# Kernel optimization log

Hardware: AMD Instinct MI355X
Metric: run time of the kernel (lower is better)

## Reference

```python
import jax, jax.numpy as jnp
import numpy as np

C = 64
EPS_LN = 1e-5
EPS_BN = 1e-5


def _conv1x1(x, w, b):
    # x: (B,C,H,W), w: (O,I), b: (O,)
    return jnp.einsum('oi,bihw->bohw', w, x) + b[None, :, None, None]


def _cross_attn(x_a, x_b, wq, bq, wk, bk, wv, bv):
    # query from x_a, key/value from x_b; residual onto x_a
    b, c, h, w = x_a.shape
    hw = h * w
    scale = 1.0 / jnp.sqrt(jnp.asarray(C, x_a.dtype))
    q = _conv1x1(x_a, wq, bq).reshape(b, -1, hw)   # (B,C,HW)
    k = _conv1x1(x_b, wk, bk).reshape(b, -1, hw)   # (B,C,HW)
    v = _conv1x1(x_b, wv, bv).reshape(b, -1, hw)   # (B,C,HW)
    # torch: bmm(k^T, q) -> (B,HW,HW), softmax over last dim
    logits = jnp.einsum('bci,bcj->bij', k, q) * scale
    attn = jax.nn.softmax(logits, axis=-1)
    out = jnp.einsum('bci,bij->bcj', v, attn).reshape(b, -1, h, w)
    return out + x_a


def _layernorm_ch(x, g, b):
    # LayerNorm over channel dim of (B,C,H,W)
    mu = jnp.mean(x, axis=1, keepdims=True)
    var = jnp.var(x, axis=1, keepdims=True)
    xn = (x - mu) * jax.lax.rsqrt(var + EPS_LN)
    return xn * g[None, :, None, None] + b[None, :, None, None]


def setup_inputs() -> dict:
    key = jax.random.key(0)
    ks = jax.random.split(key, 20)
    B, H, W = 4, 64, 64
    s = 0.05
    d = {
        'x_s2': jax.random.normal(ks[0], (B, C, H, W), jnp.float32),
        'x_dem': jax.random.normal(ks[1], (B, C, H, W), jnp.float32),
        'wq1': jax.random.normal(ks[2], (C, C), jnp.float32) * s,
        'bq1': jnp.zeros((C,), jnp.float32),
        'wk1': jax.random.normal(ks[3], (C, C), jnp.float32) * s,
        'bk1': jnp.zeros((C,), jnp.float32),
        'wv1': jax.random.normal(ks[4], (C, C), jnp.float32) * s,
        'bv1': jnp.zeros((C,), jnp.float32),
        'wq2': jax.random.normal(ks[5], (C, C), jnp.float32) * s,
        'bq2': jnp.zeros((C,), jnp.float32),
        'wk2': jax.random.normal(ks[6], (C, C), jnp.float32) * s,
        'bk2': jnp.zeros((C,), jnp.float32),
        'wv2': jax.random.normal(ks[7], (C, C), jnp.float32) * s,
        'bv2': jnp.zeros((C,), jnp.float32),
        'ln_s2_w': jnp.ones((C,), jnp.float32),
        'ln_s2_b': jnp.zeros((C,), jnp.float32),
        'ln_dem_w': jnp.ones((C,), jnp.float32),
        'ln_dem_b': jnp.zeros((C,), jnp.float32),
        'fw1': jax.random.normal(ks[8], (C, 2 * C, 3, 3), jnp.float32) * s,
        'fb1': jnp.zeros((C,), jnp.float32),
        'bn_g': jnp.ones((C,), jnp.float32),
        'bn_b': jnp.zeros((C,), jnp.float32),
        'fw2': jax.random.normal(ks[9], (C, C), jnp.float32) * s,
        'fb2': jnp.zeros((C,), jnp.float32),
    }
    return d


def reference(x_s2, x_dem, wq1, bq1, wk1, bk1, wv1, bv1,
              wq2, bq2, wk2, bk2, wv2, bv2,
              ln_s2_w, ln_s2_b, ln_dem_w, ln_dem_b,
              fw1, fb1, bn_g, bn_b, fw2, fb2):
    out_s2 = _cross_attn(x_s2, x_dem, wq1, bq1, wk1, bk1, wv1, bv1)
    out_dem = _cross_attn(x_dem, x_s2, wq2, bq2, wk2, bk2, wv2, bv2)
    out_s2 = _layernorm_ch(out_s2, ln_s2_w, ln_s2_b)
    out_dem = _layernorm_ch(out_dem, ln_dem_w, ln_dem_b)
    combined = jnp.concatenate([out_s2, out_dem], axis=1)  # (B,2C,H,W)
    y = jax.lax.conv_general_dilated(
        combined, fw1, window_strides=(1, 1), padding='SAME',
        dimension_numbers=('NCHW', 'OIHW', 'NCHW')) + fb1[None, :, None, None]
    # BatchNorm2d in training mode: batch statistics over (B,H,W)
    mu = jnp.mean(y, axis=(0, 2, 3), keepdims=True)
    var = jnp.var(y, axis=(0, 2, 3), keepdims=True)
    y = (y - mu) * jax.lax.rsqrt(var + EPS_BN)
    y = y * bn_g[None, :, None, None] + bn_b[None, :, None, None]
    y = jax.nn.relu(y)
    return _conv1x1(y, fw2, fb2)
```

## Files before the change

### kernel.cpp

```cpp
#include <hip/hip_runtime.h>
#include <hip/hip_bf16.h>


using bf16x8 = __attribute__((ext_vector_type(8))) short;
using f32x4  = __attribute__((ext_vector_type(4))) float;
using f32x16 = __attribute__((ext_vector_type(16))) float;
typedef unsigned int uint2v __attribute__((ext_vector_type(2)));

#define MFMA16(a, b, c) __builtin_amdgcn_mfma_f32_16x16x32_bf16((a), (b), (c), 0, 0, 0)
#define MFMA32(a, b, c) __builtin_amdgcn_mfma_f32_32x32x16_bf16((a), (b), (c), 0, 0, 0)

constexpr int B_ = 4, C_ = 64, S_ = 4096;
constexpr float kQS = 0.18033688f;

constexpr size_t OFF_XT   = 0;
constexpr size_t OFF_WB   = 4u * 1024 * 1024;
constexpr size_t OFF_FW1R = OFF_WB + 64 * 1024;
constexpr size_t OFF_QT   = OFF_FW1R + 160 * 1024;
constexpr size_t OFF_KT   = OFF_QT + 4u * 1024 * 1024;
constexpr size_t OFF_V    = OFF_KT + 4u * 1024 * 1024;
constexpr size_t OFF_COMB = OFF_V + 4u * 1024 * 1024;
constexpr size_t OFF_Y    = OFF_COMB + 4u * 1024 * 1024;
constexpr size_t OFF_PART = OFF_Y + 4u * 1024 * 1024;
constexpr size_t OFF_BNA  = OFF_PART + 128 * 1024;
constexpr size_t OFF_BNB  = OFF_BNA + 1024;

__device__ __forceinline__ unsigned short f2bf(float f) {
  unsigned int u = __float_as_uint(f);
  unsigned int r = (u + 0x7fffu + ((u >> 16) & 1u)) >> 16;
  return (unsigned short)r;
}
__device__ __forceinline__ unsigned int cvt_pk_bf16(float lo, float hi) {
  unsigned int r;
  asm("v_cvt_pk_bf16_f32 %0, %1, %2" : "=v"(r) : "v"(lo), "v"(hi));
  return r;
}
__device__ __forceinline__ float fast_exp2(float x) {
#if __has_builtin(__builtin_amdgcn_exp2f)
  return __builtin_amdgcn_exp2f(x);
#else
  return exp2f(x);
#endif
}
__device__ __forceinline__ void plswap(unsigned int& a, unsigned int& b) {
  uint2v r = __builtin_amdgcn_permlane32_swap(a, b, false, false);
  a = r[0];
  b = r[1];
}

__device__ __forceinline__ void build_pv_frags(const f32x16 s, float& lsum,
                                               bf16x8* out) {
  float p[16];
#pragma unroll
  for (int r = 0; r < 16; ++r) p[r] = fast_exp2(s[r]);
  lsum += (((p[0] + p[1]) + (p[2] + p[3])) + ((p[4] + p[5]) + (p[6] + p[7]))) +
          (((p[8] + p[9]) + (p[10] + p[11])) + ((p[12] + p[13]) + (p[14] + p[15])));
#pragma unroll
  for (int h = 0; h < 2; ++h) {
    unsigned int X  = cvt_pk_bf16(p[8 * h + 0], p[8 * h + 1]);
    unsigned int X2 = cvt_pk_bf16(p[8 * h + 2], p[8 * h + 3]);
    unsigned int Y  = cvt_pk_bf16(p[8 * h + 4], p[8 * h + 5]);
    unsigned int Y2 = cvt_pk_bf16(p[8 * h + 6], p[8 * h + 7]);
    plswap(X, Y);
    plswap(X2, Y2);
    union { unsigned int u[4]; bf16x8 v; } bb;
    bb.u[0] = X; bb.u[1] = X2; bb.u[2] = Y; bb.u[3] = Y2;
    out[h] = bb.v;
  }
}

__global__ void k_prep(const float* wq1, const float* wk1, const float* wv1,
                       const float* wq2, const float* wk2, const float* wv2,
                       const float* fw2, const float* fw1,
                       const float* xs2, const float* xdem,
                       unsigned short* wb, unsigned short* fw1r,
                       unsigned short* xT) {
  __shared__ float lds[64][65];
  if (blockIdx.x < 400) {
    int g = blockIdx.x * 256 + threadIdx.x;
    if (g < 7 * 4096) {
      int m = g >> 12, idx = g & 4095;
      const float* src[7] = {wq1, wk1, wv1, wq2, wk2, wv2, fw2};
      float sc = (m == 0 || m == 3) ? kQS : 1.0f;
      wb[g] = f2bf(src[m][idx] * sc);
    } else {
      int t = g - 7 * 4096;
      if (t < 64 * 1152) {
        int o = t / 1152, kk = t % 1152;
        int dydx = kk >> 7, ci = kk & 127;
        fw1r[t] = f2bf(fw1[o * 1152 + ci * 9 + dydx]);
      }
    }
    return;
  }
  int bid = blockIdx.x - 400;
  int pt = bid & 63, b = (bid >> 6) & 3, tz = bid >> 8;
  int tid = threadIdx.x;
  const float* src = (tz == 0) ? xs2 : xdem;
  int p0 = pt * 64;
#pragma unroll
  for (int k = 0; k < 16; ++k) {
    int idx = k * 256 + tid;
    int c = idx >> 6, pp = idx & 63;
    lds[c][pp] = src[((size_t)(b * 64 + c) << 12) + p0 + pp];
  }
  __syncthreads();
  unsigned short* dst = xT + (size_t)tz * (B_ * S_ * C_);
#pragma unroll
  for (int k = 0; k < 4; ++k) {
    int p = (tid >> 4) + k * 16;
    int c0 = (tid & 15) * 4;
    ushort4 v;
    v.x = f2bf(lds[c0 + 0][p]);
    v.y = f2bf(lds[c0 + 1][p]);
    v.z = f2bf(lds[c0 + 2][p]);
    v.w = f2bf(lds[c0 + 3][p]);
    *(ushort4*)&dst[((size_t)((b << 12) + p0 + p)) * 64 + c0] = v;
  }
}

__global__ __launch_bounds__(256) void k_proj(
    const unsigned short* xT, const unsigned short* wb,
    const float* bq1, const float* bk1, const float* bv1,
    const float* bq2, const float* bk2, const float* bv2,
    unsigned short* Qf, unsigned short* Kf, unsigned short* Vf) {
  int pc = blockIdx.x, b = blockIdx.y, dir = blockIdx.z;
  int lane = threadIdx.x & 63, wid = threadIdx.x >> 6;
  int l4 = lane & 15, g4 = lane >> 4;
  const unsigned short* xq =
      xT + ((size_t)(dir * B_ + b)) * (size_t)(S_ * C_);
  const unsigned short* xkv =
      xT + ((size_t)((1 - dir) * B_ + b)) * (size_t)(S_ * C_);
  size_t dbOff = ((size_t)dir * B_ + b) * (size_t)(S_ * C_);
  const float* bq = dir ? bq2 : bq1;
  const float* bk = dir ? bk2 : bk1;
  const float* bv = dir ? bv2 : bv1;
  int pbase = pc * 64 + wid * 16;

  bf16x8 aq[2], akv[2];
#pragma unroll
  for (int kc = 0; kc < 2; ++kc) {
    aq[kc] = *(const bf16x8*)&xq[(size_t)(pbase + l4) * 64 + kc * 32 + g4 * 8];
    akv[kc] = *(const bf16x8*)&xkv[(size_t)(pbase + l4) * 64 + kc * 32 + g4 * 8];
  }

#pragma unroll
  for (int prod = 0; prod < 2; ++prod) {
    const unsigned short* wm = wb + (dir * 3 + prod) * 4096;
    unsigned short* dst = (prod == 0 ? Qf : Kf) + dbOff;
    const float* bp = (prod == 0) ? bq : bk;
    float bscale = (prod == 0) ? kQS : 1.0f;
    const bf16x8* af = (prod == 0) ? aq : akv;
#pragma unroll
    for (int nt = 0; nt < 4; ++nt) {
      bf16x8 wf0 = *(const bf16x8*)&wm[(nt * 16 + l4) * 64 + g4 * 8];
      bf16x8 wf1 = *(const bf16x8*)&wm[(nt * 16 + l4) * 64 + 32 + g4 * 8];
      f32x4 acc = {0.f, 0.f, 0.f, 0.f};
      acc = MFMA16(af[0], wf0, acc);
      acc = MFMA16(af[1], wf1, acc);
      float bias_c = bp[nt * 16 + l4] * bscale;
#pragma unroll
      for (int r = 0; r < 4; ++r)
        dst[(size_t)nt * 65536 + (size_t)(pbase + g4 * 4 + r) * 16 + l4] =
            f2bf(acc[r] + bias_c);
    }
  }
  {
    const unsigned short* wm = wb + (dir * 3 + 2) * 4096;
    unsigned short* dst = Vf + dbOff;
#pragma unroll
    for (int mt = 0; mt < 4; ++mt) {
      bf16x8 wf0 = *(const bf16x8*)&wm[(mt * 16 + l4) * 64 + g4 * 8];
      bf16x8 wf1 = *(const bf16x8*)&wm[(mt * 16 + l4) * 64 + 32 + g4 * 8];
      f32x4 acc = {0.f, 0.f, 0.f, 0.f};
      acc = MFMA16(wf0, akv[0], acc);
      acc = MFMA16(wf1, akv[1], acc);
#pragma unroll
      for (int r = 0; r < 4; ++r) {
        int c = mt * 16 + g4 * 4 + r;
        dst[(size_t)(pbase >> 4) * 1024 + c * 16 + l4] = f2bf(acc[r] + bv[c]);
      }
    }
  }
}

constexpr int TST = 72;

__global__ __launch_bounds__(256, 4) void k_attn(
    const unsigned short* Qf, const unsigned short* Kf, const unsigned short* Vf,
    const float* xs2, const float* xdem,
    const float* lnw_s2, const float* lnb_s2,
    const float* lnw_dem, const float* lnb_dem,
    unsigned short* comb) {
  __shared__ __align__(16) char smem[17408];
  const f32x16 kZero16 = {0.f, 0.f, 0.f, 0.f, 0.f, 0.f, 0.f, 0.f,
                          0.f, 0.f, 0.f, 0.f, 0.f, 0.f, 0.f, 0.f};
  int bd = blockIdx.x, jb = blockIdx.y;
  int dir = bd >> 2, b = bd & 3;
  int lane = threadIdx.x & 63, wid = threadIdx.x >> 6;
  int l5 = lane & 31;
  int h = lane >> 5;
  int hi8 = h * 8, hi4 = h * 4;
  size_t dbOff = (size_t)bd * (size_t)(S_ * C_);
  const unsigned short* qp = Qf + dbOff;
  const unsigned short* kp = Kf + dbOff;
  const unsigned short* vp = Vf + dbOff;

  int jbase = jb * 32;
  bf16x8 qf[4];
#pragma unroll
  for (int kc = 0; kc < 4; ++kc)
    qf[kc] = *(const bf16x8*)&qp[(size_t)kc * 65536 + (size_t)(jbase + l5) * 16 + hi8];

  f32x16 acc0 = kZero16, acc1 = kZero16;
  float lsum = 0.f;
  int ibeg = wid * 1024;

  for (int t = 0; t < 32; ++t) {
    int i0 = ibeg + t * 32;
    bf16x8 ak[4], av[4];
#pragma unroll
    for (int k = 0; k < 4; ++k)
      ak[k] = *(const bf16x8*)&kp[(size_t)k * 65536 + (size_t)(i0 + l5) * 16 + hi8];
    int ic = i0 >> 4;
    av[0] = *(const bf16x8*)&vp[(size_t)ic * 1024 + l5 * 16 + hi8];
    av[1] = *(const bf16x8*)&vp[(size_t)(ic + 1) * 1024 + l5 * 16 + hi8];
    av[2] = *(const bf16x8*)&vp[(size_t)ic * 1024 + (32 + l5) * 16 + hi8];
    av[3] = *(const bf16x8*)&vp[(size_t)(ic + 1) * 1024 + (32 + l5) * 16 + hi8];

    f32x16 S = kZero16;
    S = MFMA32(ak[0], qf[0], S);
    S = MFMA32(ak[1], qf[1], S);
    S = MFMA32(ak[2], qf[2], S);
    S = MFMA32(ak[3], qf[3], S);
    bf16x8 pb[2];
    build_pv_frags(S, lsum, pb);
    acc0 = MFMA32(av[0], pb[0], acc0);
    acc0 = MFMA32(av[1], pb[1], acc0);
    acc1 = MFMA32(av[2], pb[0], acc1);
    acc1 = MFMA32(av[3], pb[1], acc1);
  }

  float* Lp = (float*)(smem + 16384);
  Lp[wid * 64 + lane] = lsum;

#define STORE1(A_, CIDX, RG)                                              \
  {                                                                       \
    _Pragma("unroll") for (int q2 = 0; q2 < 4; ++q2) {                    \
      f32x4 tv = {(A_)[q2 * 4 + 0], (A_)[q2 * 4 + 1],                     \
                  (A_)[q2 * 4 + 2], (A_)[q2 * 4 + 3]};                    \
      *(f32x4*)&(RG)[((CIDX) * 4 + q2) * 256 + lane * 4] = tv;            \
    }                                                                     \
  }
#define ADD1(A_, CIDX, RR)                                                \
  {                                                                       \
    _Pragma("unroll") for (int q2 = 0; q2 < 4; ++q2) {                    \
      f32x4 tv = *(const f32x4*)&(RR)[((CIDX) * 4 + q2) * 256 + lane * 4];\
      _Pragma("unroll") for (int e = 0; e < 4; ++e) (A_)[q2 * 4 + e] += tv[e]; \
    }                                                                     \
  }
#define PUB(SLOT)                                                         \
  {                                                                       \
    float* rg_ = (float*)(smem + (size_t)(SLOT) * 8192);                  \
    STORE1(acc0, 0, rg_) STORE1(acc1, 1, rg_)                             \
  }
#define ADDP(SLOT)                                                        \
  {                                                                       \
    const float* rr_ = (const float*)(smem + (size_t)(SLOT) * 8192);      \
    ADD1(acc0, 0, rr_) ADD1(acc1, 1, rr_)                                 \
  }

  if (wid >= 2) PUB(wid - 2)
  __syncthreads();
  if (wid == 1) {
    ADDP(1)
    PUB(1)
  } else if (wid == 0) {
    ADDP(0)
  }
  __syncthreads();
  if (wid != 0) return;
  ADDP(1)
#undef PUB
#undef ADDP
#undef STORE1
#undef ADD1

  float ls = 0.f;
#pragma unroll
  for (int ihh = 0; ihh < 4; ++ihh) ls += Lp[ihh * 64 + lane];
  ls += __shfl_xor(ls, 32);
  float linv = 1.0f / ls;

  const float* xa = (dir == 0 ? xs2 : xdem) + (size_t)b * C_ * S_;
  const float* lw = (dir == 0) ? lnw_s2 : lnw_dem;
  const float* lbp = (dir == 0) ? lnb_s2 : lnb_dem;
  int jcol = jbase + l5;

  float vals[32];
  float s1 = 0.f, s2 = 0.f;
#pragma unroll
  for (int ct = 0; ct < 2; ++ct)
#pragma unroll
    for (int reg = 0; reg < 16; ++reg) {
      int c = ct * 32 + (reg & 3) + 8 * (reg >> 2) + hi4;
      float v = (ct ? acc1[reg] : acc0[reg]) * linv + xa[(size_t)c * S_ + jcol];
      vals[ct * 16 + reg] = v;
      s1 += v;
      s2 += v * v;
    }
  s1 += __shfl_xor(s1, 32);
  s2 += __shfl_xor(s2, 32);
  float mean = s1 * (1.0f / 64.0f);
  float var = s2 * (1.0f / 64.0f) - mean * mean;
  float rstd = rsqrtf(var + 1e-5f);

  unsigned short* T = (unsigned short*)smem;
#pragma unroll
  for (int ct = 0; ct < 2; ++ct)
#pragma unroll
    for (int q2 = 0; q2 < 4; ++q2)
#pragma unroll
      for (int pp = 0; pp < 2; ++pp) {
        int r0 = q2 * 4 + pp * 2;
        int c0 = ct * 32 + 8 * q2 + hi4 + pp * 2;
        float x0 = (vals[ct * 16 + r0 + 0] - mean) * rstd * lw[c0 + 0] + lbp[c0 + 0];
        float x1 = (vals[ct * 16 + r0 + 1] - mean) * rstd * lw[c0 + 1] + lbp[c0 + 1];
        *(unsigned int*)&T[l5 * TST + c0] = cvt_pk_bf16(x0, x1);
      }
  int j_l = lane >> 1, cc = (lane & 1) * 32;
  unsigned short* cb =
      comb + ((size_t)b * S_ + jbase + j_l) * 128 + dir * 64 + cc;
  const unsigned short* ts = &T[j_l * TST + cc];
#pragma unroll
  for (int q = 0; q < 4; ++q) {
    uint4 tq = *(const uint4*)&ts[q * 8];
    *(uint4*)&cb[q * 8] = tq;
  }
}

__global__ __launch_bounds__(256) void k_conv3(const unsigned short* comb,
                                               const unsigned short* fw1r,
                                               const float* fb1, float* y,
                                               float* part) {
  __shared__ float red[4][128];
  int pc = blockIdx.x, b = blockIdx.y;
  int lane = threadIdx.x & 63, wid = threadIdx.x >> 6;
  int l4 = lane & 15, g4 = lane >> 4;
  int p0 = pc * 64 + wid * 16;
  int p_l = p0 + l4;
  int py0 = p_l >> 6, px0 = p_l & 63;
  f32x4 acc[4];
#pragma unroll
  for (int ot = 0; ot < 4; ++ot) acc[ot] = f32x4{0.f, 0.f, 0.f, 0.f};

#pragma unroll
  for (int kk9 = 0; kk9 < 9; ++kk9) {
    int py = py0 + (kk9 / 3) - 1;
    int px = px0 + (kk9 % 3) - 1;
    bool ok = (py >= 0) && (py < 64) && (px >= 0) && (px < 64);
    const unsigned short* base = comb + ((size_t)(b << 12) + py * 64 + px) * 128;
#pragma unroll
    for (int kc = 0; kc < 4; ++kc) {
      bf16x8 af = {0, 0, 0, 0, 0, 0, 0, 0};
      if (ok) af = *(const bf16x8*)&base[kc * 32 + g4 * 8];
#pragma unroll
      for (int ot = 0; ot < 4; ++ot) {
        bf16x8 bfr = *(const bf16x8*)&fw1r[(size_t)(ot * 16 + l4) * 1152 + kk9 * 128 + kc * 32 + g4 * 8];
        acc[ot] = MFMA16(af, bfr, acc[ot]);
      }
    }
  }
  float ps[4], ps2[4];
#pragma unroll
  for (int ot = 0; ot < 4; ++ot) {
    float bias = fb1[ot * 16 + l4];
    float s = 0.f, s2 = 0.f;
#pragma unroll
    for (int r = 0; r < 4; ++r) {
      float v = acc[ot][r] + bias;
      y[((size_t)(b << 12) + p0 + g4 * 4 + r) * 64 + ot * 16 + l4] = v;
      s += v;
      s2 += v * v;
    }
    s += __shfl_xor(s, 16);
    s += __shfl_xor(s, 32);
    s2 += __shfl_xor(s2, 16);
    s2 += __shfl_xor(s2, 32);
    ps[ot] = s;
    ps2[ot] = s2;
  }
  if (lane < 16) {
#pragma unroll
    for (int ot = 0; ot < 4; ++ot) {
      red[wid][ot * 16 + lane] = ps[ot];
      red[wid][64 + ot * 16 + lane] = ps2[ot];
    }
  }
  __syncthreads();
  if (wid == 0) {
    int o = lane;
    float s = red[0][o] + red[1][o] + red[2][o] + red[3][o];
    float s2 = red[0][64 + o] + red[1][64 + o] + red[2][64 + o] + red[3][64 + o];
    int blk = b * 64 + pc;
    part[(blk * 64 + o) * 2 + 0] = s;
    part[(blk * 64 + o) * 2 + 1] = s2;
  }
}

__global__ void k_bnfin(const float* part, const float* bng, const float* bnb,
                        float* bnA, float* bnB) {
  int o = threadIdx.x;
  float s = 0.f, s2 = 0.f;
  for (int k = 0; k < 256; ++k) {
    s += part[(k * 64 + o) * 2 + 0];
    s2 += part[(k * 64 + o) * 2 + 1];
  }
  float mean = s * (1.0f / 16384.0f);
  float var = s2 * (1.0f / 16384.0f) - mean * mean;
  float a = bng[o] * rsqrtf(var + 1e-5f);
  bnA[o] = a;
  bnB[o] = bnb[o] - mean * a;
}

__global__ __launch_bounds__(128) void k_final(const float* y, const unsigned short* fw2b,
                                               const float* bnA, const float* bnB,
                                               const float* fb2, float* out) {
  int pc = blockIdx.x, b = blockIdx.y;
  int lane = threadIdx.x & 63, wid = threadIdx.x >> 6;
  int l4 = lane & 15, g4 = lane >> 4;
  int p0 = pc * 32 + wid * 16;

  bf16x8 afw[4][2];
#pragma unroll
  for (int mt = 0; mt < 4; ++mt)
#pragma unroll
    for (int kc = 0; kc < 2; ++kc)
      afw[mt][kc] = *(const bf16x8*)&fw2b[(mt * 16 + l4) * 64 + kc * 32 + g4 * 8];
  float a8[2][8], b8[2][8];
#pragma unroll
  for (int kc = 0; kc < 2; ++kc)
#pragma unroll
    for (int e = 0; e < 8; ++e) {
      int c = kc * 32 + g4 * 8 + e;
      a8[kc][e] = bnA[c];
      b8[kc][e] = bnB[c];
    }
  float fbv[4][4];
#pragma unroll
  for (int mt = 0; mt < 4; ++mt)
#pragma unroll
    for (int r = 0; r < 4; ++r) fbv[mt][r] = fb2[mt * 16 + g4 * 4 + r];

  f32x4 acc[4];
#pragma unroll
  for (int mt = 0; mt < 4; ++mt) acc[mt] = f32x4{0.f, 0.f, 0.f, 0.f};

#pragma unroll
  for (int kc = 0; kc < 2; ++kc) {
    const float* yrow = &y[((size_t)(b << 12) + p0 + l4) * 64 + kc * 32 + g4 * 8];
    float4 y0 = *(const float4*)yrow;
    float4 y1 = *(const float4*)(yrow + 4);
    float zv[8] = {y0.x, y0.y, y0.z, y0.w, y1.x, y1.y, y1.z, y1.w};
    bf16x8 zf;
#pragma unroll
    for (int e = 0; e < 8; ++e)
      zf[e] = (short)f2bf(fmaxf(zv[e] * a8[kc][e] + b8[kc][e], 0.f));
#pragma unroll
    for (int mt = 0; mt < 4; ++mt) acc[mt] = MFMA16(afw[mt][kc], zf, acc[mt]);
  }
#pragma unroll
  for (int mt = 0; mt < 4; ++mt)
#pragma unroll
    for (int r = 0; r < 4; ++r)
      out[((size_t)b * 64 + mt * 16 + g4 * 4 + r) * (size_t)S_ + p0 + l4] =
          acc[mt][r] + fbv[mt][r];
}

extern "C" void kernel_launch(void* const* d_in, const int* in_sizes, int n_in,
                              void* d_out, int out_size, void* d_ws, size_t ws_size,
                              hipStream_t stream) {
  const float* x_s2 = (const float*)d_in[0];
  const float* x_dem = (const float*)d_in[1];
  const float* wq1 = (const float*)d_in[2];
  const float* bq1 = (const float*)d_in[3];
  const float* wk1 = (const float*)d_in[4];
  const float* bk1 = (const float*)d_in[5];
  const float* wv1 = (const float*)d_in[6];
  const float* bv1 = (const float*)d_in[7];
  const float* wq2 = (const float*)d_in[8];
  const float* bq2 = (const float*)d_in[9];
  const float* wk2 = (const float*)d_in[10];
  const float* bk2 = (const float*)d_in[11];
  const float* wv2 = (const float*)d_in[12];
  const float* bv2 = (const float*)d_in[13];
  const float* ln_s2_w = (const float*)d_in[14];
  const float* ln_s2_b = (const float*)d_in[15];
  const float* ln_dem_w = (const float*)d_in[16];
  const float* ln_dem_b = (const float*)d_in[17];
  const float* fw1 = (const float*)d_in[18];
  const float* fb1 = (const float*)d_in[19];
  const float* bn_g = (const float*)d_in[20];
  const float* bn_b = (const float*)d_in[21];
  const float* fw2 = (const float*)d_in[22];
  const float* fb2 = (const float*)d_in[23];

  char* ws = (char*)d_ws;
  unsigned short* xT = (unsigned short*)(ws + OFF_XT);
  unsigned short* wbuf = (unsigned short*)(ws + OFF_WB);
  unsigned short* fw1r = (unsigned short*)(ws + OFF_FW1R);
  unsigned short* Qf = (unsigned short*)(ws + OFF_QT);
  unsigned short* Kf = (unsigned short*)(ws + OFF_KT);
  unsigned short* Vf = (unsigned short*)(ws + OFF_V);
  unsigned short* comb = (unsigned short*)(ws + OFF_COMB);
  float* ybuf = (float*)(ws + OFF_Y);
  float* part = (float*)(ws + OFF_PART);
  float* bnA = (float*)(ws + OFF_BNA);
  float* bnB = (float*)(ws + OFF_BNB);

  k_prep<<<912, 256, 0, stream>>>(wq1, wk1, wv1, wq2, wk2, wv2, fw2, fw1,
                                  x_s2, x_dem, wbuf, fw1r, xT);
  k_proj<<<dim3(64, 4, 2), 256, 0, stream>>>(xT, wbuf, bq1, bk1, bv1,
                                             bq2, bk2, bv2, Qf, Kf, Vf);
  k_attn<<<dim3(8, 128), 256, 0, stream>>>(Qf, Kf, Vf, x_s2, x_dem,
                                           ln_s2_w, ln_s2_b, ln_dem_w, ln_dem_b,
                                           comb);
  k_conv3<<<dim3(64, 4), 256, 0, stream>>>(comb, fw1r, fb1, ybuf, part);
  k_bnfin<<<1, 64, 0, stream>>>(part, bn_g, bn_b, bnA, bnB);
  k_final<<<dim3(128, 4), 128, 0, stream>>>(ybuf, wbuf + 6 * 4096, bnA, bnB, fb2,
                                            (float*)d_out);
}
```

Before: 101.6 us.

## Process two query column groups per attention block to reuse K/V loads

```diff
diff --git a/kernel.cpp b/kernel.cpp
--- a/kernel.cpp
+++ b/kernel.cpp
@@ -186,13 +186,13 @@
 
 constexpr int TST = 72;
 
-__global__ __launch_bounds__(256, 4) void k_attn(
+__global__ __launch_bounds__(256, 2) void k_attn(
     const unsigned short* Qf, const unsigned short* Kf, const unsigned short* Vf,
     const float* xs2, const float* xdem,
     const float* lnw_s2, const float* lnb_s2,
     const float* lnw_dem, const float* lnb_dem,
     unsigned short* comb) {
-  __shared__ __align__(16) char smem[17408];
+  __shared__ __align__(16) char smem[34816];
   const f32x16 kZero16 = {0.f, 0.f, 0.f, 0.f, 0.f, 0.f, 0.f, 0.f,
                           0.f, 0.f, 0.f, 0.f, 0.f, 0.f, 0.f, 0.f};
   int bd = blockIdx.x, jb = blockIdx.y;
@@ -206,14 +206,17 @@
   const unsigned short* kp = Kf + dbOff;
   const unsigned short* vp = Vf + dbOff;
 
-  int jbase = jb * 32;
-  bf16x8 qf[4];
-#pragma unroll
-  for (int kc = 0; kc < 4; ++kc)
-    qf[kc] = *(const bf16x8*)&qp[(size_t)kc * 65536 + (size_t)(jbase + l5) * 16 + hi8];
-
-  f32x16 acc0 = kZero16, acc1 = kZero16;
-  float lsum = 0.f;
+  int jbase = jb * 64;
+  bf16x8 qf[2][4];
+#pragma unroll
+  for (int jg = 0; jg < 2; ++jg)
+#pragma unroll
+    for (int kc = 0; kc < 4; ++kc)
+      qf[jg][kc] = *(const bf16x8*)&qp[(size_t)kc * 65536 +
+                                       (size_t)(jbase + jg * 32 + l5) * 16 + hi8];
+
+  f32x16 acc00 = kZero16, acc01 = kZero16, acc10 = kZero16, acc11 = kZero16;
+  float lsum0 = 0.f, lsum1 = 0.f;
   int ibeg = wid * 1024;
 
   for (int t = 0; t < 32; ++t) {
@@ -228,21 +231,34 @@
     av[2] = *(const bf16x8*)&vp[(size_t)ic * 1024 + (32 + l5) * 16 + hi8];
     av[3] = *(const bf16x8*)&vp[(size_t)(ic + 1) * 1024 + (32 + l5) * 16 + hi8];
 
-    f32x16 S = kZero16;
-    S = MFMA32(ak[0], qf[0], S);
-    S = MFMA32(ak[1], qf[1], S);
-    S = MFMA32(ak[2], qf[2], S);
-    S = MFMA32(ak[3], qf[3], S);
-    bf16x8 pb[2];
-    build_pv_frags(S, lsum, pb);
-    acc0 = MFMA32(av[0], pb[0], acc0);
-    acc0 = MFMA32(av[1], pb[1], acc0);
-    acc1 = MFMA32(av[2], pb[0], acc1);
-    acc1 = MFMA32(av[3], pb[1], acc1);
-  }
-
-  float* Lp = (float*)(smem + 16384);
-  Lp[wid * 64 + lane] = lsum;
+    f32x16 S0 = kZero16;
+    S0 = MFMA32(ak[0], qf[0][0], S0);
+    S0 = MFMA32(ak[1], qf[0][1], S0);
+    S0 = MFMA32(ak[2], qf[0][2], S0);
+    S0 = MFMA32(ak[3], qf[0][3], S0);
+    bf16x8 pb0[2];
+    build_pv_frags(S0, lsum0, pb0);
+    f32x16 S1 = kZero16;
+    S1 = MFMA32(ak[0], qf[1][0], S1);
+    S1 = MFMA32(ak[1], qf[1][1], S1);
+    S1 = MFMA32(ak[2], qf[1][2], S1);
+    S1 = MFMA32(ak[3], qf[1][3], S1);
+    bf16x8 pb1[2];
+    build_pv_frags(S1, lsum1, pb1);
+
+    acc00 = MFMA32(av[0], pb0[0], acc00);
+    acc00 = MFMA32(av[1], pb0[1], acc00);
+    acc01 = MFMA32(av[2], pb0[0], acc01);
+    acc01 = MFMA32(av[3], pb0[1], acc01);
+    acc10 = MFMA32(av[0], pb1[0], acc10);
+    acc10 = MFMA32(av[1], pb1[1], acc10);
+    acc11 = MFMA32(av[2], pb1[0], acc11);
+    acc11 = MFMA32(av[3], pb1[1], acc11);
+  }
+
+  float* Lp = (float*)(smem + 32768);
+  Lp[wid * 128 + lane] = lsum0;
+  Lp[wid * 128 + 64 + lane] = lsum1;
 
 #define STORE1(A_, CIDX, RG)                                              \
   {                                                                       \
@@ -261,81 +277,85 @@
   }
 #define PUB(SLOT)                                                         \
   {                                                                       \
-    float* rg_ = (float*)(smem + (size_t)(SLOT) * 8192);                  \
-    STORE1(acc0, 0, rg_) STORE1(acc1, 1, rg_)                             \
+    float* rg_ = (float*)(smem + (size_t)(SLOT) * 16384);                 \
+    STORE1(acc00, 0, rg_) STORE1(acc01, 1, rg_)                           \
+    STORE1(acc10, 2, rg_) STORE1(acc11, 3, rg_)                           \
   }
 #define ADDP(SLOT)                                                        \
   {                                                                       \
-    const float* rr_ = (const float*)(smem + (size_t)(SLOT) * 8192);      \
-    ADD1(acc0, 0, rr_) ADD1(acc1, 1, rr_)                                 \
+    const float* rr_ = (const float*)(smem + (size_t)(SLOT) * 16384);     \
+    ADD1(acc00, 0, rr_) ADD1(acc01, 1, rr_)                               \
+    ADD1(acc10, 2, rr_) ADD1(acc11, 3, rr_)                               \
   }
 
   if (wid >= 2) PUB(wid - 2)
   __syncthreads();
-  if (wid == 1) {
-    ADDP(1)
-    PUB(1)
-  } else if (wid == 0) {
-    ADDP(0)
-  }
+  if (wid < 2) ADDP(wid)
+  __syncthreads();
+  if (wid == 1) PUB(0)
   __syncthreads();
   if (wid != 0) return;
-  ADDP(1)
+  ADDP(0)
 #undef PUB
 #undef ADDP
 #undef STORE1
 #undef ADD1
 
-  float ls = 0.f;
-#pragma unroll
-  for (int ihh = 0; ihh < 4; ++ihh) ls += Lp[ihh * 64 + lane];
-  ls += __shfl_xor(ls, 32);
-  float linv = 1.0f / ls;
-
   const float* xa = (dir == 0 ? xs2 : xdem) + (size_t)b * C_ * S_;
   const float* lw = (dir == 0) ? lnw_s2 : lnw_dem;
   const float* lbp = (dir == 0) ? lnb_s2 : lnb_dem;
-  int jcol = jbase + l5;
-
-  float vals[32];
-  float s1 = 0.f, s2 = 0.f;
-#pragma unroll
-  for (int ct = 0; ct < 2; ++ct)
-#pragma unroll
-    for (int reg = 0; reg < 16; ++reg) {
-      int c = ct * 32 + (reg & 3) + 8 * (reg >> 2) + hi4;
-      float v = (ct ? acc1[reg] : acc0[reg]) * linv + xa[(size_t)c * S_ + jcol];
-      vals[ct * 16 + reg] = v;
-      s1 += v;
-      s2 += v * v;
-    }
-  s1 += __shfl_xor(s1, 32);
-  s2 += __shfl_xor(s2, 32);
-  float mean = s1 * (1.0f / 64.0f);
-  float var = s2 * (1.0f / 64.0f) - mean * mean;
-  float rstd = rsqrtf(var + 1e-5f);
-
   unsigned short* T = (unsigned short*)smem;
-#pragma unroll
-  for (int ct = 0; ct < 2; ++ct)
-#pragma unroll
-    for (int q2 = 0; q2 < 4; ++q2)
-#pragma unroll
-      for (int pp = 0; pp < 2; ++pp) {
-        int r0 = q2 * 4 + pp * 2;
-        int c0 = ct * 32 + 8 * q2 + hi4 + pp * 2;
-        float x0 = (vals[ct * 16 + r0 + 0] - mean) * rstd * lw[c0 + 0] + lbp[c0 + 0];
-        float x1 = (vals[ct * 16 + r0 + 1] - mean) * rstd * lw[c0 + 1] + lbp[c0 + 1];
-        *(unsigned int*)&T[l5 * TST + c0] = cvt_pk_bf16(x0, x1);
+
+#pragma unroll
+  for (int jg = 0; jg < 2; ++jg) {
+    float ls = 0.f;
+#pragma unroll
+    for (int w = 0; w < 4; ++w) ls += Lp[w * 128 + jg * 64 + lane];
+    ls += __shfl_xor(ls, 32);
+    float linv = 1.0f / ls;
+    int jcol = jbase + jg * 32 + l5;
+
+    float vals[32];
+    float s1 = 0.f, s2 = 0.f;
+#pragma unroll
+    for (int ct = 0; ct < 2; ++ct)
+#pragma unroll
+      for (int reg = 0; reg < 16; ++reg) {
+        int c = ct * 32 + (reg & 3) + 8 * (reg >> 2) + hi4;
+        float a_ = (jg == 0) ? (ct == 0 ? acc00[reg] : acc01[reg])
+                             : (ct == 0 ? acc10[reg] : acc11[reg]);
+        float v = a_ * linv + xa[(size_t)c * S_ + jcol];
+        vals[ct * 16 + reg] = v;
+        s1 += v;
+        s2 += v * v;
       }
-  int j_l = lane >> 1, cc = (lane & 1) * 32;
-  unsigned short* cb =
-      comb + ((size_t)b * S_ + jbase + j_l) * 128 + dir * 64 + cc;
-  const unsigned short* ts = &T[j_l * TST + cc];
-#pragma unroll
-  for (int q = 0; q < 4; ++q) {
-    uint4 tq = *(const uint4*)&ts[q * 8];
-    *(uint4*)&cb[q * 8] = tq;
+    s1 += __shfl_xor(s1, 32);
+    s2 += __shfl_xor(s2, 32);
+    float mean = s1 * (1.0f / 64.0f);
+    float var = s2 * (1.0f / 64.0f) - mean * mean;
+    float rstd = rsqrtf(var + 1e-5f);
+
+#pragma unroll
+    for (int ct = 0; ct < 2; ++ct)
+#pragma unroll
+      for (int q2 = 0; q2 < 4; ++q2)
+#pragma unroll
+        for (int pp = 0; pp < 2; ++pp) {
+          int r0 = q2 * 4 + pp * 2;
+          int c0 = ct * 32 + 8 * q2 + hi4 + pp * 2;
+          float x0 = (vals[ct * 16 + r0 + 0] - mean) * rstd * lw[c0 + 0] + lbp[c0 + 0];
+          float x1 = (vals[ct * 16 + r0 + 1] - mean) * rstd * lw[c0 + 1] + lbp[c0 + 1];
+          *(unsigned int*)&T[l5 * TST + c0] = cvt_pk_bf16(x0, x1);
+        }
+    int j_l = lane >> 1, cc = (lane & 1) * 32;
+    unsigned short* cb =
+        comb + ((size_t)b * S_ + jbase + jg * 32 + j_l) * 128 + dir * 64 + cc;
+    const unsigned short* ts = &T[j_l * TST + cc];
+#pragma unroll
+    for (int q = 0; q < 4; ++q) {
+      uint4 tq = *(const uint4*)&ts[q * 8];
+      *(uint4*)&cb[q * 8] = tq;
+    }
   }
 }
 
@@ -522,9 +542,9 @@
                                   x_s2, x_dem, wbuf, fw1r, xT);
   k_proj<<<dim3(64, 4, 2), 256, 0, stream>>>(xT, wbuf, bq1, bk1, bv1,
                                              bq2, bk2, bv2, Qf, Kf, Vf);
-  k_attn<<<dim3(8, 128), 256, 0, stream>>>(Qf, Kf, Vf, x_s2, x_dem,
-                                           ln_s2_w, ln_s2_b, ln_dem_w, ln_dem_b,
-                                           comb);
+  k_attn<<<dim3(8, 64), 256, 0, stream>>>(Qf, Kf, Vf, x_s2, x_dem,
+                                          ln_s2_w, ln_s2_b, ln_dem_w, ln_dem_b,
+                                          comb);
   k_conv3<<<dim3(64, 4), 256, 0, stream>>>(comb, fw1r, fb1, ybuf, part);
   k_bnfin<<<1, 64, 0, stream>>>(part, bn_g, bn_b, bnA, bnB);
   k_final<<<dim3(128, 4), 128, 0, stream>>>(ybuf, wbuf + 6 * 4096, bnA, bnB, fb2,
```

Result: no change. 100.8 us (-0.7%).
